# Performance work log

Hardware: AMD Instinct MI355X
Metric: run time of the kernel (lower is better)

Reference implementation:

```python
import jax, jax.numpy as jnp
import numpy as np

WS = 7          # window size (odd)
NUM_HEADS = 4


def _indices(H, W, ws):
    """Replicates get_attn_idx / get_bias_idx from the torch module (static numpy)."""
    H_, W_ = H - (ws - 1), W - (ws - 1)
    pad = ws // 2
    # unfold idx: flat key indices of each ws x ws window anchored at valid positions
    h_idx = np.tile(np.arange(W_), H_)
    w_idx = np.repeat(np.arange(H_), W_) * W
    k_idx = np.tile(np.arange(ws), ws) + np.repeat(np.arange(ws), ws) * W
    unfold = (h_idx + w_idx)[:, None] + k_idx            # [H_*W_, ws^2]
    # replication-pad the map of valid-window ids to size H x W
    amap = np.arange(H_ * W_).reshape(H_, W_)
    amap = np.pad(amap, pad, mode='edge').reshape(-1)    # [H*W]
    attn_idx = unfold[amap]                              # [H*W, ws^2]
    # relative-position bias indices
    nh = np.ones(ws, dtype=np.int64); nh[pad] = H - (ws - 1)
    nw = np.ones(ws, dtype=np.int64); nw[pad] = W - (ws - 1)
    ih = np.repeat(np.arange(ws), nh)                    # [H]
    iw = np.repeat(np.arange(ws), nw)                    # [W]
    idx_k = (np.arange(ws)[:, None] * (2 * ws - 1) + np.arange(ws)).reshape(-1)
    bias_hw = ih[:, None] * (2 * ws - 1) + iw            # [H, W]
    bias_idx = (bias_hw[..., None] + idx_k).reshape(-1, ws * ws)  # [H*W, ws^2]
    return jnp.asarray(attn_idx, jnp.int32), jnp.asarray(bias_idx, jnp.int32)


def setup_inputs() -> dict:
    key = jax.random.key(0)
    ks = jax.random.split(key, 6)
    B, C, H, W = 2, 64, 128, 128
    return {
        'x': jax.random.normal(ks[0], (B, C, H, W), jnp.float32),
        'qkv_w': jax.random.normal(ks[1], (3 * C, C), jnp.float32) * 0.05,
        'qkv_b': jax.random.normal(ks[2], (3 * C,), jnp.float32) * 0.05,
        'proj_w': jax.random.normal(ks[3], (C, C), jnp.float32) * 0.05,
        'proj_b': jax.random.normal(ks[4], (C,), jnp.float32) * 0.05,
        'relative_bias': jax.random.normal(ks[5], ((2 * WS - 1) ** 2, NUM_HEADS), jnp.float32) * 0.02,
    }


def reference(x, qkv_w, qkv_b, proj_w, proj_b, relative_bias):
    B, C, H, W = x.shape
    nH = NUM_HEADS
    hd = C // nH
    scale = hd ** -0.5
    attn_idx, bias_idx = _indices(H, W, WS)   # static int constants

    # 1x1 conv qkv
    qkv = jnp.einsum('bchw,oc->bohw', x, qkv_w) + qkv_b[None, :, None, None]
    qkv = qkv.reshape(B, 3, nH, hd, H * W)
    q = qkv[:, 0].transpose(0, 1, 3, 2) * scale          # [B,nH,HW,hd]
    k = qkv[:, 1].transpose(0, 1, 3, 2)
    v = qkv[:, 2].transpose(0, 1, 3, 2)

    kg = k[:, :, attn_idx]                               # [B,nH,HW,ws^2,hd]
    bias = relative_bias[bias_idx].transpose(2, 0, 1)    # [nH,HW,ws^2]
    attn = jnp.einsum('bhnd,bhnkd->bhnk', q, kg) + bias[None]
    attn = jax.nn.softmax(attn, axis=-1)

    out = jnp.einsum('bhnk,bhnkd->bhnd', attn, v[:, :, attn_idx])  # [B,nH,HW,hd]
    out = out.transpose(0, 1, 3, 2).reshape(B, C, H, W)

    out = jnp.einsum('bchw,oc->bohw', out, proj_w) + proj_b[None, :, None, None]
    return out
```

## Files before the change

### kernel.cpp

```cpp
#include <hip/hip_runtime.h>

#define HW 16384
#define NH 4
#define HD 16

__global__ __launch_bounds__(256) void qkv_kernel(
    const float* __restrict__ x, const float* __restrict__ w,
    const float* __restrict__ bias, float* __restrict__ qT,
    float* __restrict__ kT, float* __restrict__ vT)
{
  __shared__ float xs[64][72];
  int slice = blockIdx.x;
  int p0    = blockIdx.y * 64;
  int b     = blockIdx.z;
  int t     = threadIdx.x;

  {
    int c = t >> 2, f4 = t & 3;
    const float4* src = (const float4*)(x + (size_t)(b * 64 + c) * HW + p0);
    float4* dst = (float4*)(&xs[c][0]);
#pragma unroll
    for (int k2 = 0; k2 < 4; ++k2) dst[f4 * 4 + k2] = src[f4 * 4 + k2];
  }
  __syncthreads();

  int px = t & 63;
  int wv  = __builtin_amdgcn_readfirstlane(t >> 6);
  int o16 = slice * 4 + wv;
  int o0  = o16 * 16;
  int tsel = o16 >> 2;
  int h    = o16 & 3;

  float acc[16];
#pragma unroll
  for (int d = 0; d < 16; ++d) acc[d] = bias[o0 + d];

  for (int c4 = 0; c4 < 16; ++c4) {
    float a0 = xs[c4 * 4 + 0][px];
    float a1 = xs[c4 * 4 + 1][px];
    float a2 = xs[c4 * 4 + 2][px];
    float a3 = xs[c4 * 4 + 3][px];
#pragma unroll
    for (int d = 0; d < 16; ++d) {
      const float* wr = w + (o0 + d) * 64 + c4 * 4;
      acc[d] = fmaf(wr[0], a0, acc[d]);
      acc[d] = fmaf(wr[1], a1, acc[d]);
      acc[d] = fmaf(wr[2], a2, acc[d]);
      acc[d] = fmaf(wr[3], a3, acc[d]);
    }
  }
  if (tsel == 0) {
#pragma unroll
    for (int d = 0; d < 16; ++d) acc[d] *= 0.25f;
  }
  float* dst = (tsel == 0) ? qT : ((tsel == 1) ? kT : vT);
  float4* dp = (float4*)(dst + ((size_t)(b * NH + h) * HW + p0 + px) * HD);
  dp[0] = make_float4(acc[0], acc[1], acc[2], acc[3]);
  dp[1] = make_float4(acc[4], acc[5], acc[6], acc[7]);
  dp[2] = make_float4(acc[8], acc[9], acc[10], acc[11]);
  dp[3] = make_float4(acc[12], acc[13], acc[14], acc[15]);
}

__global__ __launch_bounds__(256) void attn_kernel(
    const float* __restrict__ qT, const float* __restrict__ kT,
    const float* __restrict__ vT, const float* __restrict__ rb,
    float* __restrict__ attO)
{
  __shared__ float Kl[16][22][22];
  __shared__ float Vl[16][22][22];
  __shared__ float rbl[169];

  int tile = blockIdx.x;
  int h    = blockIdx.y;
  int b    = blockIdx.z;
  int tx0  = (tile & 7) * 16;
  int ty0  = (tile >> 3) * 16;
  int oy   = ty0 - 3, ox = tx0 - 3;
  int t    = threadIdx.x;

  size_t base = (size_t)(b * NH + h) * HW;

  if (t < 169) rbl[t] = rb[t * NH + h];

  for (int idx = t; idx < 1936; idx += 256) {
    int pxi = idx >> 2, d4 = idx & 3;
    int r = pxi / 22, c = pxi % 22;
    int ra = oy + r; ra = ra < 0 ? 0 : (ra > 127 ? 127 : ra);
    int ca = ox + c; ca = ca < 0 ? 0 : (ca > 127 ? 127 : ca);
    size_t gp = (base + (size_t)ra * 128 + ca) * HD;
    float4 kv = ((const float4*)(kT + gp))[d4];
    float4 vv = ((const float4*)(vT + gp))[d4];
    int dd = d4 * 4;
    Kl[dd + 0][r][c] = kv.x; Kl[dd + 1][r][c] = kv.y;
    Kl[dd + 2][r][c] = kv.z; Kl[dd + 3][r][c] = kv.w;
    Vl[dd + 0][r][c] = vv.x; Vl[dd + 1][r][c] = vv.y;
    Vl[dd + 2][r][c] = vv.z; Vl[dd + 3][r][c] = vv.w;
  }

  int lx = t & 15, ly = t >> 4;
  int y = ty0 + ly, xc = tx0 + lx;
  int sy = y - 3;  sy = sy < 0 ? 0 : (sy > 121 ? 121 : sy);
  int sx = xc - 3; sx = sx < 0 ? 0 : (sx > 121 ? 121 : sx);
  int li0 = sy - oy, lj0 = sx - ox;
  int ih = y - sy, iw = xc - sx;

  float qd[16];
  {
    const float4* qp = (const float4*)(qT + (base + (size_t)y * 128 + xc) * HD);
#pragma unroll
    for (int k = 0; k < 4; ++k) {
      float4 v = qp[k];
      qd[4 * k + 0] = v.x; qd[4 * k + 1] = v.y;
      qd[4 * k + 2] = v.z; qd[4 * k + 3] = v.w;
    }
  }

  __syncthreads();

  float lg[49];
#pragma unroll
  for (int i = 0; i < 7; ++i) {
#pragma unroll
    for (int j = 0; j < 7; ++j) {
      int r = li0 + i, c = lj0 + j;
      float d = 0.f;
#pragma unroll
      for (int dd = 0; dd < 16; ++dd) d = fmaf(qd[dd], Kl[dd][r][c], d);
      lg[i * 7 + j] = d + rbl[(ih + i) * 13 + (iw + j)];
    }
  }

  float mx = lg[0];
#pragma unroll
  for (int k = 1; k < 49; ++k) mx = fmaxf(mx, lg[k]);
  float s = 0.f;
#pragma unroll
  for (int k = 0; k < 49; ++k) { lg[k] = __expf(lg[k] - mx); s += lg[k]; }
  float inv = 1.f / s;

  float o[16];
#pragma unroll
  for (int dd = 0; dd < 16; ++dd) o[dd] = 0.f;
#pragma unroll
  for (int i = 0; i < 7; ++i) {
#pragma unroll
    for (int j = 0; j < 7; ++j) {
      int r = li0 + i, c = lj0 + j;
      float p = lg[i * 7 + j];
#pragma unroll
      for (int dd = 0; dd < 16; ++dd) o[dd] = fmaf(p, Vl[dd][r][c], o[dd]);
    }
  }

  size_t op = (size_t)y * 128 + xc;
#pragma unroll
  for (int dd = 0; dd < 16; ++dd)
    attO[((size_t)b * 64 + h * 16 + dd) * HW + op] = o[dd] * inv;
}

__global__ __launch_bounds__(256) void proj_kernel(
    const float* __restrict__ pw, const float* __restrict__ pb,
    float* __restrict__ out)
{
  __shared__ float as[64][72];
  int p0 = blockIdx.x * 64;
  int b  = blockIdx.y;
  int t  = threadIdx.x;

  {
    int c = t >> 2, f4 = t & 3;
    const float4* src = (const float4*)(out + (size_t)(b * 64 + c) * HW + p0);
    float4* dst = (float4*)(&as[c][0]);
#pragma unroll
    for (int k2 = 0; k2 < 4; ++k2) dst[f4 * 4 + k2] = src[f4 * 4 + k2];
  }
  __syncthreads();

  int px = t & 63;
  int og = __builtin_amdgcn_readfirstlane(t >> 6);
  float acc[16];
#pragma unroll
  for (int oo = 0; oo < 16; ++oo) acc[oo] = pb[og * 16 + oo];

  for (int c4 = 0; c4 < 16; ++c4) {
    float a0 = as[c4 * 4 + 0][px];
    float a1 = as[c4 * 4 + 1][px];
    float a2 = as[c4 * 4 + 2][px];
    float a3 = as[c4 * 4 + 3][px];
#pragma unroll
    for (int oo = 0; oo < 16; ++oo) {
      const float* wr = pw + (og * 16 + oo) * 64 + c4 * 4;
      acc[oo] = fmaf(wr[0], a0, acc[oo]);
      acc[oo] = fmaf(wr[1], a1, acc[oo]);
      acc[oo] = fmaf(wr[2], a2, acc[oo]);
      acc[oo] = fmaf(wr[3], a3, acc[oo]);
    }
  }
#pragma unroll
  for (int oo = 0; oo < 16; ++oo)
    out[((size_t)b * 64 + og * 16 + oo) * HW + p0 + px] = acc[oo];
}

extern "C" void kernel_launch(void* const* d_in, const int* in_sizes, int n_in,
                              void* d_out, int out_size, void* d_ws, size_t ws_size,
                              hipStream_t stream) {
  const float* x      = (const float*)d_in[0];
  const float* qkv_w  = (const float*)d_in[1];
  const float* qkv_b  = (const float*)d_in[2];
  const float* proj_w = (const float*)d_in[3];
  const float* proj_b = (const float*)d_in[4];
  const float* rb     = (const float*)d_in[5];
  float* out = (float*)d_out;

  const size_t TSZ = (size_t)2 * NH * HW * HD;
  float* qT = (float*)d_ws;
  float* kT = qT + TSZ;
  float* vT = kT + TSZ;

  qkv_kernel<<<dim3(3, 256, 2), 256, 0, stream>>>(x, qkv_w, qkv_b, qT, kT, vT);
  attn_kernel<<<dim3(64, NH, 2), 256, 0, stream>>>(qT, kT, vT, rb, out);
  proj_kernel<<<dim3(256, 2), 256, 0, stream>>>(proj_w, proj_b, out);
}
```

Before: 67.51 us.

## Use swizzled pixel-major float4 LDS layout and reuse one buffer for K then V

The attention kernel now stores each K/V pixel's 16 channels contiguously in shared memory, using an XOR swizzle. This lets the dot products and weighted sums use four 128-bit LDS reads per neighbour instead of sixteen scalar reads, and the transposing scalar stores during staging go away. K and V now share a single buffer: V is loaded after the logits are computed, with two extra barriers. That halves shared memory, which may raise occupancy, but the V load is serialized after the QK phase instead of overlapping with it.

```diff
diff --git a/kernel.cpp b/kernel.cpp
--- a/kernel.cpp
+++ b/kernel.cpp
@@ -61,13 +61,22 @@
   dp[3] = make_float4(acc[12], acc[13], acc[14], acc[15]);
 }
 
+
+__device__ __forceinline__ float4* swzp(float* buf, int px, int d4) {
+  int off = (px << 6) ^ (((px & 7) ^ d4) << 4);
+  return (float4*)((char*)buf + off);
+}
+__device__ __forceinline__ const float4* swzpc(const float* buf, int px, int d4) {
+  int off = (px << 6) ^ (((px & 7) ^ d4) << 4);
+  return (const float4*)((const char*)buf + off);
+}
+
 __global__ __launch_bounds__(256) void attn_kernel(
     const float* __restrict__ qT, const float* __restrict__ kT,
     const float* __restrict__ vT, const float* __restrict__ rb,
     float* __restrict__ attO)
 {
-  __shared__ float Kl[16][22][22];
-  __shared__ float Vl[16][22][22];
+  __shared__ float KV[484 * 16];
   __shared__ float rbl[169];
 
   int tile = blockIdx.x;
@@ -88,13 +97,7 @@
     int ra = oy + r; ra = ra < 0 ? 0 : (ra > 127 ? 127 : ra);
     int ca = ox + c; ca = ca < 0 ? 0 : (ca > 127 ? 127 : ca);
     size_t gp = (base + (size_t)ra * 128 + ca) * HD;
-    float4 kv = ((const float4*)(kT + gp))[d4];
-    float4 vv = ((const float4*)(vT + gp))[d4];
-    int dd = d4 * 4;
-    Kl[dd + 0][r][c] = kv.x; Kl[dd + 1][r][c] = kv.y;
-    Kl[dd + 2][r][c] = kv.z; Kl[dd + 3][r][c] = kv.w;
-    Vl[dd + 0][r][c] = vv.x; Vl[dd + 1][r][c] = vv.y;
-    Vl[dd + 2][r][c] = vv.z; Vl[dd + 3][r][c] = vv.w;
+    *swzp(KV, pxi, d4) = ((const float4*)(kT + gp))[d4];
   }
 
   int lx = t & 15, ly = t >> 4;
@@ -122,11 +125,22 @@
   for (int i = 0; i < 7; ++i) {
 #pragma unroll
     for (int j = 0; j < 7; ++j) {
-      int r = li0 + i, c = lj0 + j;
-      float d = 0.f;
-#pragma unroll
-      for (int dd = 0; dd < 16; ++dd) d = fmaf(qd[dd], Kl[dd][r][c], d);
-      lg[i * 7 + j] = d + rbl[(ih + i) * 13 + (iw + j)];
+      int px = (li0 + i) * 22 + (lj0 + j);
+      float4 k0 = *swzpc(KV, px, 0);
+      float4 k1 = *swzpc(KV, px, 1);
+      float4 k2 = *swzpc(KV, px, 2);
+      float4 k3 = *swzpc(KV, px, 3);
+      float d;
+      d = fmaf(qd[0], k0.x, rbl[(ih + i) * 13 + (iw + j)]);
+      d = fmaf(qd[1], k0.y, d);  d = fmaf(qd[2], k0.z, d);
+      d = fmaf(qd[3], k0.w, d);  d = fmaf(qd[4], k1.x, d);
+      d = fmaf(qd[5], k1.y, d);  d = fmaf(qd[6], k1.z, d);
+      d = fmaf(qd[7], k1.w, d);  d = fmaf(qd[8], k2.x, d);
+      d = fmaf(qd[9], k2.y, d);  d = fmaf(qd[10], k2.z, d);
+      d = fmaf(qd[11], k2.w, d); d = fmaf(qd[12], k3.x, d);
+      d = fmaf(qd[13], k3.y, d); d = fmaf(qd[14], k3.z, d);
+      d = fmaf(qd[15], k3.w, d);
+      lg[i * 7 + j] = d;
     }
   }
 
@@ -138,24 +152,49 @@
   for (int k = 0; k < 49; ++k) { lg[k] = __expf(lg[k] - mx); s += lg[k]; }
   float inv = 1.f / s;
 
-  float o[16];
-#pragma unroll
-  for (int dd = 0; dd < 16; ++dd) o[dd] = 0.f;
+  __syncthreads();
+  for (int idx = t; idx < 1936; idx += 256) {
+    int pxi = idx >> 2, d4 = idx & 3;
+    int r = pxi / 22, c = pxi % 22;
+    int ra = oy + r; ra = ra < 0 ? 0 : (ra > 127 ? 127 : ra);
+    int ca = ox + c; ca = ca < 0 ? 0 : (ca > 127 ? 127 : ca);
+    size_t gp = (base + (size_t)ra * 128 + ca) * HD;
+    *swzp(KV, pxi, d4) = ((const float4*)(vT + gp))[d4];
+  }
+  __syncthreads();
+
+  float4 o0 = make_float4(0,0,0,0), o1 = o0, o2 = o0, o3 = o0;
 #pragma unroll
   for (int i = 0; i < 7; ++i) {
 #pragma unroll
     for (int j = 0; j < 7; ++j) {
-      int r = li0 + i, c = lj0 + j;
+      int px = (li0 + i) * 22 + (lj0 + j);
       float p = lg[i * 7 + j];
-#pragma unroll
-      for (int dd = 0; dd < 16; ++dd) o[dd] = fmaf(p, Vl[dd][r][c], o[dd]);
+      float4 v0 = *swzpc(KV, px, 0);
+      float4 v1 = *swzpc(KV, px, 1);
+      float4 v2 = *swzpc(KV, px, 2);
+      float4 v3 = *swzpc(KV, px, 3);
+      o0.x = fmaf(p, v0.x, o0.x); o0.y = fmaf(p, v0.y, o0.y);
+      o0.z = fmaf(p, v0.z, o0.z); o0.w = fmaf(p, v0.w, o0.w);
+      o1.x = fmaf(p, v1.x, o1.x); o1.y = fmaf(p, v1.y, o1.y);
+      o1.z = fmaf(p, v1.z, o1.z); o1.w = fmaf(p, v1.w, o1.w);
+      o2.x = fmaf(p, v2.x, o2.x); o2.y = fmaf(p, v2.y, o2.y);
+      o2.z = fmaf(p, v2.z, o2.z); o2.w = fmaf(p, v2.w, o2.w);
+      o3.x = fmaf(p, v3.x, o3.x); o3.y = fmaf(p, v3.y, o3.y);
+      o3.z = fmaf(p, v3.z, o3.z); o3.w = fmaf(p, v3.w, o3.w);
     }
   }
 
   size_t op = (size_t)y * 128 + xc;
-#pragma unroll
-  for (int dd = 0; dd < 16; ++dd)
-    attO[((size_t)b * 64 + h * 16 + dd) * HW + op] = o[dd] * inv;
+  float* ob = attO + (size_t)b * 64 * HW + (size_t)h * 16 * HW + op;
+  ob[0 * HW] = o0.x * inv;  ob[1 * HW] = o0.y * inv;
+  ob[2 * HW] = o0.z * inv;  ob[3 * HW] = o0.w * inv;
+  ob[4 * HW] = o1.x * inv;  ob[5 * HW] = o1.y * inv;
+  ob[6 * HW] = o1.z * inv;  ob[7 * HW] = o1.w * inv;
+  ob[8 * HW] = o2.x * inv;  ob[9 * HW] = o2.y * inv;
+  ob[10 * HW] = o2.z * inv; ob[11 * HW] = o2.w * inv;
+  ob[12 * HW] = o3.x * inv; ob[13 * HW] = o3.y * inv;
+  ob[14 * HW] = o3.z * inv; ob[15 * HW] = o3.w * inv;
 }
 
 __global__ __launch_bounds__(256) void proj_kernel(
```

Measured after the change: 68.27 us. Within noise of the previous version (+1.1%).

## Split each query's 49 keys across four waves with split-softmax merge

Applied to the files above, without the earlier changes.

The attention kernel stops staging K/V halos in shared memory. Each pixel's 49-key window is split across four wavefronts (12 or 13 keys each), and K/V rows are read straight from global memory as float4. Per-wave max and sum are merged through shared memory, and the partial outputs are reduced in an LDS buffer before a coalesced store. The grid grows fourfold and launch bounds target higher occupancy. In exchange, it relies on cache reuse of overlapping global K/V reads instead of explicit shared staging, and adds extra syncs.

```diff
diff --git a/kernel.cpp b/kernel.cpp
--- a/kernel.cpp
+++ b/kernel.cpp
@@ -61,101 +61,127 @@
   dp[3] = make_float4(acc[12], acc[13], acc[14], acc[15]);
 }
 
-__global__ __launch_bounds__(256) void attn_kernel(
+
+#define DOT16Q(LGI, KPTR, RBV)                                          \
+  { const float4* kp = (const float4*)(KPTR);                           \
+    float4 k0 = kp[0], k1 = kp[1], k2 = kp[2], k3 = kp[3];              \
+    float dd = (RBV);                                                   \
+    dd = fmaf(qd[0], k0.x, dd);  dd = fmaf(qd[1], k0.y, dd);            \
+    dd = fmaf(qd[2], k0.z, dd);  dd = fmaf(qd[3], k0.w, dd);            \
+    dd = fmaf(qd[4], k1.x, dd);  dd = fmaf(qd[5], k1.y, dd);            \
+    dd = fmaf(qd[6], k1.z, dd);  dd = fmaf(qd[7], k1.w, dd);            \
+    dd = fmaf(qd[8], k2.x, dd);  dd = fmaf(qd[9], k2.y, dd);            \
+    dd = fmaf(qd[10], k2.z, dd); dd = fmaf(qd[11], k2.w, dd);           \
+    dd = fmaf(qd[12], k3.x, dd); dd = fmaf(qd[13], k3.y, dd);           \
+    dd = fmaf(qd[14], k3.z, dd); dd = fmaf(qd[15], k3.w, dd);           \
+    lg[LGI] = dd; }
+
+#define PVACC(LGI, VPTR)                                                \
+  { const float4* vp = (const float4*)(VPTR);                           \
+    float4 v0 = vp[0], v1 = vp[1], v2 = vp[2], v3 = vp[3];              \
+    float p = lg[LGI];                                                  \
+    o[0] = fmaf(p, v0.x, o[0]);   o[1] = fmaf(p, v0.y, o[1]);           \
+    o[2] = fmaf(p, v0.z, o[2]);   o[3] = fmaf(p, v0.w, o[3]);           \
+    o[4] = fmaf(p, v1.x, o[4]);   o[5] = fmaf(p, v1.y, o[5]);           \
+    o[6] = fmaf(p, v1.z, o[6]);   o[7] = fmaf(p, v1.w, o[7]);           \
+    o[8] = fmaf(p, v2.x, o[8]);   o[9] = fmaf(p, v2.y, o[9]);           \
+    o[10] = fmaf(p, v2.z, o[10]); o[11] = fmaf(p, v2.w, o[11]);         \
+    o[12] = fmaf(p, v3.x, o[12]); o[13] = fmaf(p, v3.y, o[13]);         \
+    o[14] = fmaf(p, v3.z, o[14]); o[15] = fmaf(p, v3.w, o[15]); }
+
+__global__ __launch_bounds__(256, 5) void attn_kernel(
     const float* __restrict__ qT, const float* __restrict__ kT,
     const float* __restrict__ vT, const float* __restrict__ rb,
     float* __restrict__ attO)
 {
-  __shared__ float Kl[16][22][22];
-  __shared__ float Vl[16][22][22];
   __shared__ float rbl[169];
-
-  int tile = blockIdx.x;
-  int h    = blockIdx.y;
-  int b    = blockIdx.z;
-  int tx0  = (tile & 7) * 16;
-  int ty0  = (tile >> 3) * 16;
-  int oy   = ty0 - 3, ox = tx0 - 3;
-  int t    = threadIdx.x;
-
-  size_t base = (size_t)(b * NH + h) * HW;
-
-  if (t < 169) rbl[t] = rb[t * NH + h];
-
-  for (int idx = t; idx < 1936; idx += 256) {
-    int pxi = idx >> 2, d4 = idx & 3;
-    int r = pxi / 22, c = pxi % 22;
-    int ra = oy + r; ra = ra < 0 ? 0 : (ra > 127 ? 127 : ra);
-    int ca = ox + c; ca = ca < 0 ? 0 : (ca > 127 ? 127 : ca);
-    size_t gp = (base + (size_t)ra * 128 + ca) * HD;
-    float4 kv = ((const float4*)(kT + gp))[d4];
-    float4 vv = ((const float4*)(vT + gp))[d4];
-    int dd = d4 * 4;
-    Kl[dd + 0][r][c] = kv.x; Kl[dd + 1][r][c] = kv.y;
-    Kl[dd + 2][r][c] = kv.z; Kl[dd + 3][r][c] = kv.w;
-    Vl[dd + 0][r][c] = vv.x; Vl[dd + 1][r][c] = vv.y;
-    Vl[dd + 2][r][c] = vv.z; Vl[dd + 3][r][c] = vv.w;
-  }
-
-  int lx = t & 15, ly = t >> 4;
-  int y = ty0 + ly, xc = tx0 + lx;
+  __shared__ float lsm[64][5];
+  __shared__ float lss[64][5];
+  __shared__ float obuf[4][64][17];
+
+  int t  = threadIdx.x;
+  int px = t & 63;
+  int s  = __builtin_amdgcn_readfirstlane(t >> 6);
+  int h  = blockIdx.y;
+  int b  = blockIdx.z;
+  int n  = blockIdx.x * 64 + px;
+  int y  = n >> 7, xc = n & 127;
   int sy = y - 3;  sy = sy < 0 ? 0 : (sy > 121 ? 121 : sy);
   int sx = xc - 3; sx = sx < 0 ? 0 : (sx > 121 ? 121 : sx);
-  int li0 = sy - oy, lj0 = sx - ox;
   int ih = y - sy, iw = xc - sx;
+
+  if (t < 169) rbl[t] = rb[t * NH + h];
+  __syncthreads();
+
+  size_t base = (size_t)(b * NH + h) * HW;
 
   float qd[16];
   {
-    const float4* qp = (const float4*)(qT + (base + (size_t)y * 128 + xc) * HD);
-#pragma unroll
-    for (int k = 0; k < 4; ++k) {
-      float4 v = qp[k];
-      qd[4 * k + 0] = v.x; qd[4 * k + 1] = v.y;
-      qd[4 * k + 2] = v.z; qd[4 * k + 3] = v.w;
-    }
-  }
-
-  __syncthreads();
-
-  float lg[49];
-#pragma unroll
-  for (int i = 0; i < 7; ++i) {
-#pragma unroll
-    for (int j = 0; j < 7; ++j) {
-      int r = li0 + i, c = lj0 + j;
-      float d = 0.f;
-#pragma unroll
-      for (int dd = 0; dd < 16; ++dd) d = fmaf(qd[dd], Kl[dd][r][c], d);
-      lg[i * 7 + j] = d + rbl[(ih + i) * 13 + (iw + j)];
-    }
-  }
-
-  float mx = lg[0];
-#pragma unroll
-  for (int k = 1; k < 49; ++k) mx = fmaxf(mx, lg[k]);
-  float s = 0.f;
-#pragma unroll
-  for (int k = 0; k < 49; ++k) { lg[k] = __expf(lg[k] - mx); s += lg[k]; }
-  float inv = 1.f / s;
+    const float4* qp = (const float4*)(qT + (base + n) * HD);
+    float4 a = qp[0], b4 = qp[1], c = qp[2], dv = qp[3];
+    qd[0] = a.x;  qd[1] = a.y;  qd[2] = a.z;  qd[3] = a.w;
+    qd[4] = b4.x; qd[5] = b4.y; qd[6] = b4.z; qd[7] = b4.w;
+    qd[8] = c.x;  qd[9] = c.y;  qd[10] = c.z; qd[11] = c.w;
+    qd[12] = dv.x; qd[13] = dv.y; qd[14] = dv.z; qd[15] = dv.w;
+  }
+
+  const float* kwin = kT + (base + (size_t)sy * 128 + sx) * HD;
+  const float* vwin = vT + (base + (size_t)sy * 128 + sx) * HD;
+  int kbase = s * 12;
+
+  float lg[13];
+#pragma unroll
+  for (int kk = 0; kk < 12; ++kk) {
+    int key = kbase + kk;
+    int ro  = key / 7;
+    int j   = key - ro * 7;
+    DOT16Q(kk, kwin + ((size_t)ro * 128 + j) * HD, rbl[(ih + ro) * 13 + iw + j]);
+  }
+  if (s == 0) {
+    DOT16Q(12, kwin + ((size_t)6 * 128 + 6) * HD, rbl[(ih + 6) * 13 + iw + 6]);
+  } else {
+    lg[12] = -1e30f;
+  }
+
+  float m_s = lg[0];
+#pragma unroll
+  for (int k = 1; k < 13; ++k) m_s = fmaxf(m_s, lg[k]);
+  float s_s = 0.f;
+#pragma unroll
+  for (int k = 0; k < 13; ++k) { lg[k] = __expf(lg[k] - m_s); s_s += lg[k]; }
+  lsm[px][s] = m_s;
+  lss[px][s] = s_s;
+  __syncthreads();
+
+  float m0 = lsm[px][0], m1 = lsm[px][1], m2 = lsm[px][2], m3 = lsm[px][3];
+  float mg = fmaxf(fmaxf(m0, m1), fmaxf(m2, m3));
+  float tot = lss[px][0] * __expf(m0 - mg) + lss[px][1] * __expf(m1 - mg)
+            + lss[px][2] * __expf(m2 - mg) + lss[px][3] * __expf(m3 - mg);
+  float fac = __expf(m_s - mg) / tot;
 
   float o[16];
 #pragma unroll
-  for (int dd = 0; dd < 16; ++dd) o[dd] = 0.f;
-#pragma unroll
-  for (int i = 0; i < 7; ++i) {
-#pragma unroll
-    for (int j = 0; j < 7; ++j) {
-      int r = li0 + i, c = lj0 + j;
-      float p = lg[i * 7 + j];
-#pragma unroll
-      for (int dd = 0; dd < 16; ++dd) o[dd] = fmaf(p, Vl[dd][r][c], o[dd]);
-    }
-  }
-
-  size_t op = (size_t)y * 128 + xc;
-#pragma unroll
-  for (int dd = 0; dd < 16; ++dd)
-    attO[((size_t)b * 64 + h * 16 + dd) * HW + op] = o[dd] * inv;
+  for (int d = 0; d < 16; ++d) o[d] = 0.f;
+#pragma unroll
+  for (int kk = 0; kk < 12; ++kk) {
+    int key = kbase + kk;
+    int ro  = key / 7;
+    int j   = key - ro * 7;
+    PVACC(kk, vwin + ((size_t)ro * 128 + j) * HD);
+  }
+  if (s == 0) { PVACC(12, vwin + ((size_t)6 * 128 + 6) * HD); }
+
+#pragma unroll
+  for (int d = 0; d < 16; ++d) obuf[s][px][d] = o[d] * fac;
+  __syncthreads();
+
+  float* ob = attO + (size_t)(b * 64 + h * 16 + s * 4) * HW + n;
+#pragma unroll
+  for (int i = 0; i < 4; ++i) {
+    int d = s * 4 + i;
+    float v = obuf[0][px][d] + obuf[1][px][d] + obuf[2][px][d] + obuf[3][px][d];
+    ob[(size_t)i * HW] = v;
+  }
 }
 
 __global__ __launch_bounds__(256) void proj_kernel(
@@ -218,6 +244,6 @@
   float* vT = kT + TSZ;
 
   qkv_kernel<<<dim3(3, 256, 2), 256, 0, stream>>>(x, qkv_w, qkv_b, qT, kT, vT);
-  attn_kernel<<<dim3(64, NH, 2), 256, 0, stream>>>(qT, kT, vT, rb, out);
+  attn_kernel<<<dim3(256, NH, 2), 256, 0, stream>>>(qT, kT, vT, rb, out);
   proj_kernel<<<dim3(256, 2), 256, 0, stream>>>(proj_w, proj_b, out);
 }
```

New measurement: 189.7 us. 181% more time.

## Split head dim across 4 lanes and read K/V windows directly from global

Applied to the files above, without the earlier changes.

The attention kernel no longer stages a 22x22 halo tile of K and V in shared memory. Instead, each pixel is handled by 4 lanes, and each lane owns 4 of the 16 head dimensions. Each lane reads its float4 slice of K and V straight from global memory and combines the partial dot products with lane shuffles. This removes the large LDS footprint and the staging loop, cuts per-thread registers so more waves can run, and quadruples the grid. The cost is that the 49-element neighbour reuse now relies on L1/L2 caching rather than LDS, and each logit needs two shuffles.

```diff
diff --git a/kernel.cpp b/kernel.cpp
--- a/kernel.cpp
+++ b/kernel.cpp
@@ -61,72 +61,47 @@
   dp[3] = make_float4(acc[12], acc[13], acc[14], acc[15]);
 }
 
-__global__ __launch_bounds__(256) void attn_kernel(
+__global__ __launch_bounds__(256, 4) void attn_kernel(
     const float* __restrict__ qT, const float* __restrict__ kT,
     const float* __restrict__ vT, const float* __restrict__ rb,
     float* __restrict__ attO)
 {
-  __shared__ float Kl[16][22][22];
-  __shared__ float Vl[16][22][22];
   __shared__ float rbl[169];
 
-  int tile = blockIdx.x;
-  int h    = blockIdx.y;
-  int b    = blockIdx.z;
-  int tx0  = (tile & 7) * 16;
-  int ty0  = (tile >> 3) * 16;
-  int oy   = ty0 - 3, ox = tx0 - 3;
-  int t    = threadIdx.x;
+  int t  = threadIdx.x;
+  int g  = t & 3;
+  int pl = t >> 2;
+  int h  = blockIdx.y;
+  int b  = blockIdx.z;
+  int n  = blockIdx.x * 64 + pl;
+  int y  = n >> 7, xc = n & 127;
+  int sy = y - 3;  sy = sy < 0 ? 0 : (sy > 121 ? 121 : sy);
+  int sx = xc - 3; sx = sx < 0 ? 0 : (sx > 121 ? 121 : sx);
+  int ih = y - sy, iw = xc - sx;
+
+  if (t < 169) rbl[t] = rb[t * NH + h];
+  __syncthreads();
 
   size_t base = (size_t)(b * NH + h) * HW;
 
-  if (t < 169) rbl[t] = rb[t * NH + h];
+  float4 qd = *(const float4*)(qT + (base + n) * HD + 4 * g);
 
-  for (int idx = t; idx < 1936; idx += 256) {
-    int pxi = idx >> 2, d4 = idx & 3;
-    int r = pxi / 22, c = pxi % 22;
-    int ra = oy + r; ra = ra < 0 ? 0 : (ra > 127 ? 127 : ra);
-    int ca = ox + c; ca = ca < 0 ? 0 : (ca > 127 ? 127 : ca);
-    size_t gp = (base + (size_t)ra * 128 + ca) * HD;
-    float4 kv = ((const float4*)(kT + gp))[d4];
-    float4 vv = ((const float4*)(vT + gp))[d4];
-    int dd = d4 * 4;
-    Kl[dd + 0][r][c] = kv.x; Kl[dd + 1][r][c] = kv.y;
-    Kl[dd + 2][r][c] = kv.z; Kl[dd + 3][r][c] = kv.w;
-    Vl[dd + 0][r][c] = vv.x; Vl[dd + 1][r][c] = vv.y;
-    Vl[dd + 2][r][c] = vv.z; Vl[dd + 3][r][c] = vv.w;
-  }
-
-  int lx = t & 15, ly = t >> 4;
-  int y = ty0 + ly, xc = tx0 + lx;
-  int sy = y - 3;  sy = sy < 0 ? 0 : (sy > 121 ? 121 : sy);
-  int sx = xc - 3; sx = sx < 0 ? 0 : (sx > 121 ? 121 : sx);
-  int li0 = sy - oy, lj0 = sx - ox;
-  int ih = y - sy, iw = xc - sx;
-
-  float qd[16];
-  {
-    const float4* qp = (const float4*)(qT + (base + (size_t)y * 128 + xc) * HD);
-#pragma unroll
-    for (int k = 0; k < 4; ++k) {
-      float4 v = qp[k];
-      qd[4 * k + 0] = v.x; qd[4 * k + 1] = v.y;
-      qd[4 * k + 2] = v.z; qd[4 * k + 3] = v.w;
-    }
-  }
-
-  __syncthreads();
+  const float* kwin = kT + (base + (size_t)sy * 128 + sx) * HD + 4 * g;
+  const float* vwin = vT + (base + (size_t)sy * 128 + sx) * HD + 4 * g;
 
   float lg[49];
 #pragma unroll
   for (int i = 0; i < 7; ++i) {
 #pragma unroll
     for (int j = 0; j < 7; ++j) {
-      int r = li0 + i, c = lj0 + j;
-      float d = 0.f;
-#pragma unroll
-      for (int dd = 0; dd < 16; ++dd) d = fmaf(qd[dd], Kl[dd][r][c], d);
-      lg[i * 7 + j] = d + rbl[(ih + i) * 13 + (iw + j)];
+      float4 kf = *(const float4*)(kwin + ((size_t)i * 128 + j) * HD);
+      float p = qd.x * kf.x;
+      p = fmaf(qd.y, kf.y, p);
+      p = fmaf(qd.z, kf.z, p);
+      p = fmaf(qd.w, kf.w, p);
+      p += __shfl_xor(p, 1, 4);
+      p += __shfl_xor(p, 2, 4);
+      lg[i * 7 + j] = p + rbl[(ih + i) * 13 + (iw + j)];
     }
   }
 
@@ -138,24 +113,25 @@
   for (int k = 0; k < 49; ++k) { lg[k] = __expf(lg[k] - mx); s += lg[k]; }
   float inv = 1.f / s;
 
-  float o[16];
-#pragma unroll
-  for (int dd = 0; dd < 16; ++dd) o[dd] = 0.f;
+  float4 o = make_float4(0.f, 0.f, 0.f, 0.f);
 #pragma unroll
   for (int i = 0; i < 7; ++i) {
 #pragma unroll
     for (int j = 0; j < 7; ++j) {
-      int r = li0 + i, c = lj0 + j;
+      float4 vf = *(const float4*)(vwin + ((size_t)i * 128 + j) * HD);
       float p = lg[i * 7 + j];
-#pragma unroll
-      for (int dd = 0; dd < 16; ++dd) o[dd] = fmaf(p, Vl[dd][r][c], o[dd]);
+      o.x = fmaf(p, vf.x, o.x);
+      o.y = fmaf(p, vf.y, o.y);
+      o.z = fmaf(p, vf.z, o.z);
+      o.w = fmaf(p, vf.w, o.w);
     }
   }
 
-  size_t op = (size_t)y * 128 + xc;
-#pragma unroll
-  for (int dd = 0; dd < 16; ++dd)
-    attO[((size_t)b * 64 + h * 16 + dd) * HW + op] = o[dd] * inv;
+  float* ob = attO + (size_t)(b * 64 + h * 16 + 4 * g) * HW + n;
+  ob[0]          = o.x * inv;
+  ob[(size_t)HW]     = o.y * inv;
+  ob[(size_t)2 * HW] = o.z * inv;
+  ob[(size_t)3 * HW] = o.w * inv;
 }
 
 __global__ __launch_bounds__(256) void proj_kernel(
@@ -218,6 +194,6 @@
   float* vT = kT + TSZ;
 
   qkv_kernel<<<dim3(3, 256, 2), 256, 0, stream>>>(x, qkv_w, qkv_b, qT, kT, vT);
-  attn_kernel<<<dim3(64, NH, 2), 256, 0, stream>>>(qT, kT, vT, rb, out);
+  attn_kernel<<<dim3(256, NH, 2), 256, 0, stream>>>(qT, kT, vT, rb, out);
   proj_kernel<<<dim3(256, 2), 256, 0, stream>>>(proj_w, proj_b, out);
 }
```

Result: slower. 72.78 us (+7.8%).
